# Kernel tuning notes

Measured on AMD Instinct MI355X. Metric: run time of the kernel, lower is better.

Reference implementation:

```python
import jax, jax.numpy as jnp
from jax import lax
import numpy as np

N_ITERS = 1000
LR = 0.1
EPS = 1e-8


def _log_mag_loss(sos, target_dB):
    """MSE between 20*log10(|sosfreqz(sos)|) and target_dB (matches LogMagTargetFrequencyLoss)."""
    n = target_dB.shape[-1]
    w = jnp.linspace(0.0, np.pi, n)            # [n] freqs in [0, pi]
    z1 = jnp.exp(-1j * w.astype(jnp.complex64))  # e^{-jw}, [n]
    z2 = z1 * z1                               # e^{-2jw}
    b = sos[:, :3].astype(jnp.complex64)       # [16,3] numerator coeffs
    a = sos[:, 3:].astype(jnp.complex64)       # [16,3] denominator coeffs
    # per-section response: (b0 + b1 z^-1 + b2 z^-2) / (a0 + a1 z^-1 + a2 z^-2), [16,n]
    B = b[:, 0:1] + b[:, 1:2] * z1[None, :] + b[:, 2:3] * z2[None, :]
    A = a[:, 0:1] + a[:, 1:2] * z1[None, :] + a[:, 2:3] * z2[None, :]
    H = jnp.prod(B / A, axis=0)                # cascade of sections, [n]
    mag = jnp.sqrt(jnp.real(H) ** 2 + jnp.imag(H) ** 2)
    input_dB = 20.0 * jnp.log10(mag + EPS)
    return jnp.mean((input_dB - target_dB) ** 2)


def setup_inputs() -> dict:
    key = jax.random.key(0)
    k1, k2 = jax.random.split(key)
    sos_init = jax.random.uniform(k1, (16, 6), dtype=jnp.float32)  # torch.rand(16,6)
    target_dB = jax.random.normal(k2, (512,), dtype=jnp.float32) * 6.0  # dB-scale target curve
    return {"sos_init": sos_init, "target_dB": target_dB}


def reference(sos_init, target_dB):
    grad_fn = jax.grad(_log_mag_loss)

    def step(sos, _):
        g = grad_fn(sos, target_dB)
        return sos - LR * g, None  # plain SGD step (no momentum)

    sos_final, _ = lax.scan(step, sos_init, None, length=N_ITERS)
    return sos_final
```

## Files before the change

kernel.cpp:

```cpp
#include <hip/hip_runtime.h>
#include <math.h>

#define TPB 1024

typedef float v2f __attribute__((ext_vector_type(2)));

static __device__ __forceinline__ v2f mk2(float x, float y) {
    v2f r; r.x = x; r.y = y; return r;
}
static __device__ __forceinline__ v2f fma2(v2f a, v2f b, v2f c) {
    return __builtin_elementwise_fma(a, b, c);
}
static __device__ __forceinline__ v2f rcp2(v2f x) {
    v2f r;
    r.x = __builtin_amdgcn_rcpf(x.x);
    r.y = __builtin_amdgcn_rcpf(x.y);
    return r;
}

static __device__ __forceinline__ void quad_allsum2(float& a, float& b) {
    asm("s_nop 1\n\t"
        "v_add_f32 %0, %0, %0 quad_perm:[1,0,3,2] row_mask:0xf bank_mask:0xf bound_ctrl:0\n\t"
        "v_add_f32 %1, %1, %1 quad_perm:[1,0,3,2] row_mask:0xf bank_mask:0xf bound_ctrl:0\n\t"
        "s_nop 0\n\t"
        "v_add_f32 %0, %0, %0 quad_perm:[2,3,0,1] row_mask:0xf bank_mask:0xf bound_ctrl:0\n\t"
        "v_add_f32 %1, %1, %1 quad_perm:[2,3,0,1] row_mask:0xf bank_mask:0xf bound_ctrl:0"
        : "+v"(a), "+v"(b));
}

__device__ __forceinline__ void red6_s8(float i0, float i1, float i2,
                                        float i3, float i4, float i5,
                                        float& o0, float& o1, float& o2,
                                        float& o3, float& o4, float& o5) {
    asm("s_nop 1\n\t"
        "v_add_f32 %0, %6, %6  row_shr:8 row_mask:0xf bank_mask:0xf bound_ctrl:0\n\t"
        "v_add_f32 %3, %9, %9  row_shr:8 row_mask:0xf bank_mask:0xf bound_ctrl:0\n\t"
        "v_add_f32 %1, %7, %7  row_shr:8 row_mask:0xf bank_mask:0xf bound_ctrl:0\n\t"
        "v_add_f32 %4, %10, %10 row_shr:8 row_mask:0xf bank_mask:0xf bound_ctrl:0\n\t"
        "v_add_f32 %2, %8, %8  row_shr:8 row_mask:0xf bank_mask:0xf bound_ctrl:0\n\t"
        "v_add_f32 %5, %11, %11 row_shr:8 row_mask:0xf bank_mask:0xf bound_ctrl:0"
        : "=&v"(o0), "=&v"(o1), "=&v"(o2), "=&v"(o3), "=&v"(o4), "=&v"(o5)
        : "v"(i0), "v"(i1), "v"(i2), "v"(i3), "v"(i4), "v"(i5));
}

__device__ __forceinline__ float red1_g8(float g) {
    asm("s_nop 1\n\t"
        "v_add_f32 %0, %0, %0 row_shr:1 row_mask:0xf bank_mask:0xf bound_ctrl:0\n\t"
        "s_nop 1\n\t"
        "v_add_f32 %0, %0, %0 row_shr:2 row_mask:0xf bank_mask:0xf bound_ctrl:0\n\t"
        "s_nop 1\n\t"
        "v_add_f32 %0, %0, %0 row_shr:4 row_mask:0xf bank_mask:0xf bound_ctrl:0"
        : "+v"(g));
    return g;
}

__device__ __forceinline__ int cmap(int k) {
    return (k < 3) ? 2 * k : 2 * k - 5;
}

#define GPAD 100

__global__
__attribute__((amdgpu_flat_work_group_size(TPB, TPB), amdgpu_waves_per_eu(4, 4)))
void sgd_filter(const float* __restrict__ sos_in,
                const float* __restrict__ target,
                float* __restrict__ out) {
    __shared__ __align__(16) float sos[96];
    __shared__ __align__(16) float gpart[128][GPAD];

    const int tid = threadIdx.x;
    const int qd  = tid >> 2;
    const int pos = tid & 3;
    const float* secbase = &sos[pos * 24];

    if (tid < 96) sos[(tid / 6) * 6 + cmap(tid % 6)] = sos_in[tid];

    const int u    = tid >> 3;
    const int oct  = tid & 7;
    const int usec = u / 6, uk = u % 6;
    const int uscol = usec * 6 + cmap(uk);
    const bool upd = (tid < 768);
    const bool writer = upd && (oct == 7);
    float myc = 0.0f;
    if (writer) myc = sos_in[u];
    const float* urp = &gpart[oct][0] + u;

    const double step = 3.14159265358979323846 / 511.0;
    const float w0 = (float)((double)(2 * qd) * step);
    const float w1 = (float)((double)(2 * qd + 1) * step);
    const float c10 = cosf(w0), s10 = -sinf(w0);
    const float c20 = c10 * c10 - s10 * s10, s20 = 2.0f * c10 * s10;
    const float c11 = cosf(w1), s11 = -sinf(w1);
    const float c21 = c11 * c11 - s11 * s11, s21 = 2.0f * c11 * s11;
    const float2 tg = *(const float2*)&target[2 * qd];
    const float KC = 40.0f / (512.0f * 2.302585092994046f);

    const v2f c1v0 = mk2(c10, c10), s1v0 = mk2(s10, s10);
    const v2f c2v0 = mk2(c20, c20), s2v0 = mk2(s20, s20);
    const v2f c1v1 = mk2(c11, c11), s1v1 = mk2(s11, s11);
    const v2f c2v1 = mk2(c21, c21), s2v1 = mk2(s21, s21);

    __syncthreads();

    v2f RA0, RA1, RA2, RA3, IA0, IA1, IA2, IA3, VA0, VA1, VA2, VA3;
    v2f RB0, RB1, RB2, RB3, IB0, IB1, IB2, IB3, VB0, VB1, VB2, VB3;
    v2f NA0, NA1, NA2, NA3, NB0, NB1, NB2, NB3;

#define SEC_EVAL(sl, BA0, BA1, BA2)                                         \
    {                                                                       \
        const v2f ba0 = BA0, ba1 = BA1, ba2 = BA2;                          \
        RA##sl = fma2(ba2, c2v0, fma2(ba1, c1v0, ba0));                     \
        IA##sl = fma2(ba2, s2v0, ba1 * s1v0);                               \
        NA##sl = fma2(RA##sl, RA##sl, IA##sl * IA##sl);                     \
        RB##sl = fma2(ba2, c2v1, fma2(ba1, c1v1, ba0));                     \
        IB##sl = fma2(ba2, s2v1, ba1 * s1v1);                               \
        NB##sl = fma2(RB##sl, RB##sl, IB##sl * IB##sl);                     \
    }

#define SEC_BWD(sl)                                                         \
    {                                                                       \
        const v2f KA = KK0 * VA##sl;                                        \
        const v2f PA = KA * RA##sl;                                         \
        const v2f QA = KA * IA##sl;                                         \
        const v2f KB = KK1 * VB##sl;                                        \
        const v2f PB = KB * RB##sl;                                         \
        const v2f QB = KB * IB##sl;                                         \
        const v2f P  = PA + PB;                                             \
        const v2f G1 = fma2(c1v0, PA, s1v0 * QA) + fma2(c1v1, PB, s1v1 * QB);\
        const v2f G2 = fma2(c2v0, PA, s2v0 * QA) + fma2(c2v1, PB, s2v1 * QB);\
        float g0, g1, g2, g3, g4, g5;                                       \
        red6_s8(P.x, G1.x, G2.x, P.y, G1.y, G2.y,                           \
                g0, g1, g2, g3, g4, g5);                                    \
        if ((tid & 15) >= 8) {                                              \
            float* p = &gpart[((tid >> 4) << 1) | ((tid >> 2) & 1)]         \
                             [24 * pos + 6 * (sl)];                         \
            *(float4*)p       = make_float4(g0, g1, g2, g3);                \
            *(float2*)(p + 4) = make_float2(g4, g5);                        \
        }                                                                   \
    }

    for (int it = 0; it < 1000; ++it) {
        const float4 q0 = *(const float4*)(secbase + 0);
        const float4 q1 = *(const float4*)(secbase + 4);
        const float4 q2 = *(const float4*)(secbase + 8);
        const float4 q3 = *(const float4*)(secbase + 12);
        const float4 q4 = *(const float4*)(secbase + 16);
        const float4 q5 = *(const float4*)(secbase + 20);
        SEC_EVAL(0, mk2(q0.x, q0.y), mk2(q0.z, q0.w), mk2(q1.x, q1.y))
        SEC_EVAL(1, mk2(q1.z, q1.w), mk2(q2.x, q2.y), mk2(q2.z, q2.w))
        SEC_EVAL(2, mk2(q3.x, q3.y), mk2(q3.z, q3.w), mk2(q4.x, q4.y))
        SEC_EVAL(3, mk2(q4.z, q4.w), mk2(q5.x, q5.y), mk2(q5.z, q5.w))

        const v2f tA01 = NA0 * NA1, tA23 = NA2 * NA3;
        const v2f mA   = tA01 * tA23;
        const v2f iA   = rcp2(mA);
        const v2f iA01 = iA * tA23, iA23 = iA * tA01;
        VA0 = iA01 * NA1; VA1 = iA01 * NA0;
        VA2 = iA23 * NA3; VA3 = iA23 * NA2;
        const v2f tB01 = NB0 * NB1, tB23 = NB2 * NB3;
        const v2f mB   = tB01 * tB23;
        const v2f iB   = rcp2(mB);
        const v2f iB01 = iB * tB23, iB23 = iB * tB01;
        VB0 = iB01 * NB1; VB1 = iB01 * NB0;
        VB2 = iB23 * NB3; VB3 = iB23 * NB2;

        float L0 = __builtin_amdgcn_logf(mA.x) - __builtin_amdgcn_logf(mA.y);
        float L1 = __builtin_amdgcn_logf(mB.x) - __builtin_amdgcn_logf(mB.y);

        quad_allsum2(L0, L1);

        const float mag0   = __builtin_amdgcn_exp2f(0.5f * L0);
        const float magpe0 = mag0 + 1e-8f;
        const float indB0  = 6.020599913279624f * __builtin_amdgcn_logf(magpe0);
        const float K0 = KC * (indB0 - tg.x) * mag0 * __builtin_amdgcn_rcpf(magpe0);
        const float mag1   = __builtin_amdgcn_exp2f(0.5f * L1);
        const float magpe1 = mag1 + 1e-8f;
        const float indB1  = 6.020599913279624f * __builtin_amdgcn_logf(magpe1);
        const float K1 = KC * (indB1 - tg.y) * mag1 * __builtin_amdgcn_rcpf(magpe1);
        const v2f KK0 = mk2(K0, -K0);
        const v2f KK1 = mk2(K1, -K1);

        SEC_BWD(0) SEC_BWD(1) SEC_BWD(2) SEC_BWD(3)
        __syncthreads();

        if (upd) {
            const float r0  = urp[0],        r1  = urp[1 * 800];
            const float r2  = urp[2 * 800],  r3  = urp[3 * 800];
            const float r4  = urp[4 * 800],  r5  = urp[5 * 800];
            const float r6  = urp[6 * 800],  r7  = urp[7 * 800];
            const float r8  = urp[8 * 800],  r9  = urp[9 * 800];
            const float r10 = urp[10 * 800], r11 = urp[11 * 800];
            const float r12 = urp[12 * 800], r13 = urp[13 * 800];
            const float r14 = urp[14 * 800], r15 = urp[15 * 800];
            const float t0 = (r0 + r1) + (r2 + r3);
            const float t1 = (r4 + r5) + (r6 + r7);
            const float t2 = (r8 + r9) + (r10 + r11);
            const float t3 = (r12 + r13) + (r14 + r15);
            float g = red1_g8((t0 + t1) + (t2 + t3));
            if (writer) {
                myc = fmaf(-0.1f, g, myc);
                sos[uscol] = myc;
            }
        }
        __syncthreads();
    }

    if (writer) out[u] = myc;
}

extern "C" void kernel_launch(void* const* d_in, const int* in_sizes, int n_in,
                              void* d_out, int out_size, void* d_ws, size_t ws_size,
                              hipStream_t stream) {
    const float* sos_in = (const float*)d_in[0];
    const float* target = (const float*)d_in[1];
    float* outp = (float*)d_out;
    hipLaunchKernelGGL(sgd_filter, dim3(1), dim3(TPB), 0, stream, sos_in, target, outp);
}
```

Measured before the change: 2.014 ms.

## Restructure gradient partial layout and reduction to vectorized 32-lane DPP sums

Changes the shared-memory layout of gradient partials so each update thread reads four float4 rows instead of sixteen scalar loads, then reduces across 32 lanes with interleaved DPP adds including a row_bcast step. All 1024 threads now take part in the update, and owners update four coefficients at once. It also folds the K scaling into the per-section weights and replaces two logs with one log of a product. This trades fewer LDS loads for a longer DPP chain and padded rows.

```diff
diff --git a/kernel.cpp b/kernel.cpp
--- a/kernel.cpp
+++ b/kernel.cpp
@@ -43,22 +43,37 @@
         : "v"(i0), "v"(i1), "v"(i2), "v"(i3), "v"(i4), "v"(i5));
 }
 
-__device__ __forceinline__ float red1_g8(float g) {
+__device__ __forceinline__ void red4_g32(float& a, float& b,
+                                         float& c, float& d) {
     asm("s_nop 1\n\t"
         "v_add_f32 %0, %0, %0 row_shr:1 row_mask:0xf bank_mask:0xf bound_ctrl:0\n\t"
-        "s_nop 1\n\t"
+        "v_add_f32 %1, %1, %1 row_shr:1 row_mask:0xf bank_mask:0xf bound_ctrl:0\n\t"
+        "v_add_f32 %2, %2, %2 row_shr:1 row_mask:0xf bank_mask:0xf bound_ctrl:0\n\t"
+        "v_add_f32 %3, %3, %3 row_shr:1 row_mask:0xf bank_mask:0xf bound_ctrl:0\n\t"
         "v_add_f32 %0, %0, %0 row_shr:2 row_mask:0xf bank_mask:0xf bound_ctrl:0\n\t"
-        "s_nop 1\n\t"
-        "v_add_f32 %0, %0, %0 row_shr:4 row_mask:0xf bank_mask:0xf bound_ctrl:0"
-        : "+v"(g));
-    return g;
+        "v_add_f32 %1, %1, %1 row_shr:2 row_mask:0xf bank_mask:0xf bound_ctrl:0\n\t"
+        "v_add_f32 %2, %2, %2 row_shr:2 row_mask:0xf bank_mask:0xf bound_ctrl:0\n\t"
+        "v_add_f32 %3, %3, %3 row_shr:2 row_mask:0xf bank_mask:0xf bound_ctrl:0\n\t"
+        "v_add_f32 %0, %0, %0 row_shr:4 row_mask:0xf bank_mask:0xf bound_ctrl:0\n\t"
+        "v_add_f32 %1, %1, %1 row_shr:4 row_mask:0xf bank_mask:0xf bound_ctrl:0\n\t"
+        "v_add_f32 %2, %2, %2 row_shr:4 row_mask:0xf bank_mask:0xf bound_ctrl:0\n\t"
+        "v_add_f32 %3, %3, %3 row_shr:4 row_mask:0xf bank_mask:0xf bound_ctrl:0\n\t"
+        "v_add_f32 %0, %0, %0 row_shr:8 row_mask:0xf bank_mask:0xf bound_ctrl:0\n\t"
+        "v_add_f32 %1, %1, %1 row_shr:8 row_mask:0xf bank_mask:0xf bound_ctrl:0\n\t"
+        "v_add_f32 %2, %2, %2 row_shr:8 row_mask:0xf bank_mask:0xf bound_ctrl:0\n\t"
+        "v_add_f32 %3, %3, %3 row_shr:8 row_mask:0xf bank_mask:0xf bound_ctrl:0\n\t"
+        "v_add_f32 %0, %0, %0 row_bcast:15 row_mask:0xa bank_mask:0xf\n\t"
+        "v_add_f32 %1, %1, %1 row_bcast:15 row_mask:0xa bank_mask:0xf\n\t"
+        "v_add_f32 %2, %2, %2 row_bcast:15 row_mask:0xa bank_mask:0xf\n\t"
+        "v_add_f32 %3, %3, %3 row_bcast:15 row_mask:0xa bank_mask:0xf"
+        : "+v"(a), "+v"(b), "+v"(c), "+v"(d));
 }
 
 __device__ __forceinline__ int cmap(int k) {
     return (k < 3) ? 2 * k : 2 * k - 5;
 }
 
-#define GPAD 100
+#define GPAD 132
 
 __global__
 __attribute__((amdgpu_flat_work_group_size(TPB, TPB), amdgpu_waves_per_eu(4, 4)))
@@ -75,15 +90,22 @@
 
     if (tid < 96) sos[(tid / 6) * 6 + cmap(tid % 6)] = sos_in[tid];
 
-    const int u    = tid >> 3;
-    const int oct  = tid & 7;
-    const int usec = u / 6, uk = u % 6;
-    const int uscol = usec * 6 + cmap(uk);
-    const bool upd = (tid < 768);
-    const bool writer = upd && (oct == 7);
-    float myc = 0.0f;
-    if (writer) myc = sos_in[u];
-    const float* urp = &gpart[oct][0] + u;
+    const int c    = tid >> 5;
+    const int j    = tid & 31;
+    const int slot = c >> 1;
+    const int h    = c & 1;
+    const int us   = 4 * (slot & 3) + (slot >> 2);
+    const bool owner = ((tid & 31) == 31);
+    const float* urp = &gpart[j][4 * c];
+    float k0 = 0.f, k1 = 0.f, k2 = 0.f, k3 = 0.f;
+    if (owner) {
+        if (h == 0) {
+            k0 = sos_in[6 * us + 0]; k1 = sos_in[6 * us + 3];
+            k2 = sos_in[6 * us + 1]; k3 = sos_in[6 * us + 4];
+        } else {
+            k0 = sos_in[6 * us + 2]; k1 = sos_in[6 * us + 5];
+        }
+    }
 
     const double step = 3.14159265358979323846 / 511.0;
     const float w0 = (float)((double)(2 * qd) * step);
@@ -102,8 +124,8 @@
 
     __syncthreads();
 
-    v2f RA0, RA1, RA2, RA3, IA0, IA1, IA2, IA3, VA0, VA1, VA2, VA3;
-    v2f RB0, RB1, RB2, RB3, IB0, IB1, IB2, IB3, VB0, VB1, VB2, VB3;
+    v2f RA0, RA1, RA2, RA3, IA0, IA1, IA2, IA3;
+    v2f RB0, RB1, RB2, RB3, IB0, IB1, IB2, IB3;
     v2f NA0, NA1, NA2, NA3, NB0, NB1, NB2, NB3;
 
 #define SEC_EVAL(sl, BA0, BA1, BA2)                                         \
@@ -119,12 +141,10 @@
 
 #define SEC_BWD(sl)                                                         \
     {                                                                       \
-        const v2f KA = KK0 * VA##sl;                                        \
-        const v2f PA = KA * RA##sl;                                         \
-        const v2f QA = KA * IA##sl;                                         \
-        const v2f KB = KK1 * VB##sl;                                        \
-        const v2f PB = KB * RB##sl;                                         \
-        const v2f QB = KB * IB##sl;                                         \
+        const v2f PA = WA##sl * RA##sl;                                     \
+        const v2f QA = WA##sl * IA##sl;                                     \
+        const v2f PB = WB##sl * RB##sl;                                     \
+        const v2f QB = WB##sl * IB##sl;                                     \
         const v2f P  = PA + PB;                                             \
         const v2f G1 = fma2(c1v0, PA, s1v0 * QA) + fma2(c1v1, PB, s1v1 * QB);\
         const v2f G2 = fma2(c2v0, PA, s2v0 * QA) + fma2(c2v1, PB, s2v1 * QB);\
@@ -133,9 +153,9 @@
                 g0, g1, g2, g3, g4, g5);                                    \
         if ((tid & 15) >= 8) {                                              \
             float* p = &gpart[((tid >> 4) << 1) | ((tid >> 2) & 1)]         \
-                             [24 * pos + 6 * (sl)];                         \
-            *(float4*)p       = make_float4(g0, g1, g2, g3);                \
-            *(float2*)(p + 4) = make_float2(g4, g5);                        \
+                             [8 * (4 * (sl) + pos)];                        \
+            *(float4*)p       = make_float4(g0, g3, g1, g4);                \
+            *(float4*)(p + 4) = make_float4(g2, g5, 0.0f, 0.0f);            \
         }                                                                   \
     }
 
@@ -154,18 +174,11 @@
         const v2f tA01 = NA0 * NA1, tA23 = NA2 * NA3;
         const v2f mA   = tA01 * tA23;
         const v2f iA   = rcp2(mA);
-        const v2f iA01 = iA * tA23, iA23 = iA * tA01;
-        VA0 = iA01 * NA1; VA1 = iA01 * NA0;
-        VA2 = iA23 * NA3; VA3 = iA23 * NA2;
         const v2f tB01 = NB0 * NB1, tB23 = NB2 * NB3;
         const v2f mB   = tB01 * tB23;
         const v2f iB   = rcp2(mB);
-        const v2f iB01 = iB * tB23, iB23 = iB * tB01;
-        VB0 = iB01 * NB1; VB1 = iB01 * NB0;
-        VB2 = iB23 * NB3; VB3 = iB23 * NB2;
-
-        float L0 = __builtin_amdgcn_logf(mA.x) - __builtin_amdgcn_logf(mA.y);
-        float L1 = __builtin_amdgcn_logf(mB.x) - __builtin_amdgcn_logf(mB.y);
+        float L0 = __builtin_amdgcn_logf(mA.x * iA.y);
+        float L1 = __builtin_amdgcn_logf(mB.x * iB.y);
 
         quad_allsum2(L0, L1);
 
@@ -180,32 +193,52 @@
         const v2f KK0 = mk2(K0, -K0);
         const v2f KK1 = mk2(K1, -K1);
 
+        const v2f jA   = KK0 * iA;
+        const v2f jA01 = jA * tA23, jA23 = jA * tA01;
+        const v2f WA0 = jA01 * NA1, WA1 = jA01 * NA0;
+        const v2f WA2 = jA23 * NA3, WA3 = jA23 * NA2;
+        const v2f jB   = KK1 * iB;
+        const v2f jB01 = jB * tB23, jB23 = jB * tB01;
+        const v2f WB0 = jB01 * NB1, WB1 = jB01 * NB0;
+        const v2f WB2 = jB23 * NB3, WB3 = jB23 * NB2;
+
         SEC_BWD(0) SEC_BWD(1) SEC_BWD(2) SEC_BWD(3)
         __syncthreads();
 
-        if (upd) {
-            const float r0  = urp[0],        r1  = urp[1 * 800];
-            const float r2  = urp[2 * 800],  r3  = urp[3 * 800];
-            const float r4  = urp[4 * 800],  r5  = urp[5 * 800];
-            const float r6  = urp[6 * 800],  r7  = urp[7 * 800];
-            const float r8  = urp[8 * 800],  r9  = urp[9 * 800];
-            const float r10 = urp[10 * 800], r11 = urp[11 * 800];
-            const float r12 = urp[12 * 800], r13 = urp[13 * 800];
-            const float r14 = urp[14 * 800], r15 = urp[15 * 800];
-            const float t0 = (r0 + r1) + (r2 + r3);
-            const float t1 = (r4 + r5) + (r6 + r7);
-            const float t2 = (r8 + r9) + (r10 + r11);
-            const float t3 = (r12 + r13) + (r14 + r15);
-            float g = red1_g8((t0 + t1) + (t2 + t3));
-            if (writer) {
-                myc = fmaf(-0.1f, g, myc);
-                sos[uscol] = myc;
+        {
+            const float4 p0 = *(const float4*)urp;
+            const float4 p1 = *(const float4*)(urp + 32 * GPAD);
+            const float4 p2 = *(const float4*)(urp + 64 * GPAD);
+            const float4 p3 = *(const float4*)(urp + 96 * GPAD);
+            float t0 = (p0.x + p1.x) + (p2.x + p3.x);
+            float t1 = (p0.y + p1.y) + (p2.y + p3.y);
+            float t2 = (p0.z + p1.z) + (p2.z + p3.z);
+            float t3 = (p0.w + p1.w) + (p2.w + p3.w);
+            red4_g32(t0, t1, t2, t3);
+            if (owner) {
+                k0 = fmaf(-0.1f, t0, k0);
+                k1 = fmaf(-0.1f, t1, k1);
+                k2 = fmaf(-0.1f, t2, k2);
+                k3 = fmaf(-0.1f, t3, k3);
+                if (h == 0) {
+                    *(float2*)&sos[6 * us]     = make_float2(k0, k1);
+                    *(float2*)&sos[6 * us + 2] = make_float2(k2, k3);
+                } else {
+                    *(float2*)&sos[6 * us + 4] = make_float2(k0, k1);
+                }
             }
         }
         __syncthreads();
     }
 
-    if (writer) out[u] = myc;
+    if (owner) {
+        if (h == 0) {
+            out[6 * us + 0] = k0; out[6 * us + 3] = k1;
+            out[6 * us + 1] = k2; out[6 * us + 4] = k3;
+        } else {
+            out[6 * us + 2] = k0; out[6 * us + 5] = k1;
+        }
+    }
 }
 
 extern "C" void kernel_launch(void* const* d_in, const int* in_sizes, int n_in,
```

After: 2.032 ms. No clear change (+0.9%).
